# Optimization experiments

Measured on AMD Instinct MI355X. Metric: run time of the kernel, lower is better.

Reference implementation:

```python
import jax, jax.numpy as jnp
import numpy as np

B, S, D, E = 4, 1024, 1024, 4
HID = 2816  # multiple_of * ceil(int(2*4*D/3) / multiple_of), multiple_of=256
COND = 1024  # min(D, 1024)
NORM_EPS = 1e-5  # block norms
LN_EPS = 1e-5    # q_norm/k_norm default eps


def setup_inputs() -> dict:
    key = jax.random.key(0)
    ks = jax.random.split(key, 16)
    w = lambda i, shape: jax.random.normal(ks[i], shape, jnp.float32) * 0.02
    return {
        'x': jax.random.normal(ks[0], (B, S, D), jnp.float32),
        'freqs_cis': jax.random.normal(ks[1], (S, 32), jnp.float32),  # unused by the block
        'adaln_input': jax.random.normal(ks[2], (B, COND), jnp.float32),
        'wq': w(3, (D, D)), 'wk': w(4, (D, D)), 'wv': w(5, (D, D)), 'wo': w(6, (D, D)),
        'q_norm_w': jnp.ones((D,), jnp.float32), 'q_norm_b': jnp.zeros((D,), jnp.float32),
        'k_norm_w': jnp.ones((D,), jnp.float32), 'k_norm_b': jnp.zeros((D,), jnp.float32),
        'attn_norm_w': jnp.ones((D,), jnp.float32), 'attn_norm_b': jnp.zeros((D,), jnp.float32),
        'ffn_norm_w': jnp.ones((D,), jnp.float32), 'ffn_norm_b': jnp.zeros((D,), jnp.float32),
        'w1': w(7, (E, D, HID)), 'w2': w(8, (E, HID, D)), 'w3': w(9, (E, D, HID)),
        'router_w': w(10, (D, E)), 'router_b': jnp.zeros((E,), jnp.float32),
        'ada_w': w(11, (COND, 6 * D)), 'ada_b': jnp.zeros((6 * D,), jnp.float32),
    }


def _ln(x, w, b, eps):
    mu = jnp.mean(x, -1, keepdims=True)
    var = jnp.mean((x - mu) ** 2, -1, keepdims=True)
    return (x - mu) * jax.lax.rsqrt(var + eps) * w + b


def _attention(x, wq, wk, wv, wo, qn_w, qn_b, kn_w, kn_b):
    # NOTE: this module attends over the FEATURE dim (no head split, no 1/sqrt(d) scale):
    # xq,xk,xv are permuted to [B, D, S]; scores are [B, D, D].
    q = _ln(x @ wq, qn_w, qn_b, LN_EPS)
    k = _ln(x @ wk, kn_w, kn_b, LN_EPS)
    v = x @ wv
    scores = jnp.einsum('bsd,bse->bde', q, k)          # [B, D, D]
    attn = jax.nn.softmax(scores, axis=-1)
    out = jnp.einsum('bde,bse->bsd', attn, v)          # [B, S, D]
    return out @ wo


def _moe(x, w1, w2, w3, router_w, router_b):
    logits = x @ router_w + router_b                   # [B, S, E]
    # F.normalize default dim=1 -> L2-normalize along the SEQUENCE dim (faithful quirk)
    nrm = jnp.sqrt(jnp.sum(logits * logits, axis=1, keepdims=True))
    logits = logits / jnp.maximum(nrm, 1e-12)
    probs = jax.nn.softmax(logits, axis=-1)
    topw, topi = jax.lax.top_k(probs, 2)
    # dense combine weights [B,S,E]: identical math to the masked gather/scatter dispatch
    combine = jnp.sum(jax.nn.one_hot(topi, E, dtype=x.dtype) * topw[..., None], axis=-2)
    h1 = jnp.einsum('bsd,edh->ebsh', x, w1)
    h3 = jnp.einsum('bsd,edh->ebsh', x, w3)
    out_e = jnp.einsum('ebsh,ehd->ebsd', jnp.sin(h1) * h3, w2)
    moe = jnp.einsum('bse,ebsd->bsd', combine, out_e)
    avg = jnp.mean(probs, axis=0)                      # [S, E] (mean over batch dim only)
    aux = jnp.sum((1.0 / E - avg) ** 2)
    return moe, aux


def reference(x, freqs_cis, adaln_input, wq, wk, wv, wo, q_norm_w, q_norm_b, k_norm_w,
              k_norm_b, attn_norm_w, attn_norm_b, ffn_norm_w, ffn_norm_b, w1, w2, w3,
              router_w, router_b, ada_w, ada_b):
    ada = jax.nn.silu(adaln_input) @ ada_w + ada_b     # [B, 6D]
    shift_msa, scale_msa, gate_msa, shift_mlp, scale_mlp, gate_mlp = jnp.split(ada, 6, axis=1)
    h = _ln(x, attn_norm_w, attn_norm_b, NORM_EPS)
    h = h * (1.0 + scale_msa[:, None, :]) + shift_msa[:, None, :]
    x = x + gate_msa[:, None, :] * _attention(h, wq, wk, wv, wo, q_norm_w, q_norm_b, k_norm_w, k_norm_b)
    h = _ln(x, ffn_norm_w, ffn_norm_b, NORM_EPS)
    h = h * (1.0 + scale_mlp[:, None, :]) + shift_mlp[:, None, :]
    # MoE path REPLACES x (no residual, gate_mlp unused) — faithful to the source
    x, aux = _moe(h, w1, w2, w3, router_w, router_b)
    return x, aux
```

## Files before the change

kernel.cpp:

```cpp
#include <hip/hip_runtime.h>
#include <hip/hip_bf16.h>
#include <math.h>

#define BB 4
#define SS 1024
#define DD 1024
#define EE 4
#define HID 2816
#define HC 1408
#define SIXD 6144
#define NSLOT 8704
#define NMB 68

typedef __bf16 v8bf __attribute__((ext_vector_type(8)));
typedef float  v4f  __attribute__((ext_vector_type(4)));

__device__ __forceinline__ ushort f2bf(float f) {
    union { float f; unsigned u; } v; v.f = f;
    unsigned r = v.u + 0x7fff + ((v.u >> 16) & 1);
    return (ushort)(r >> 16);
}
__device__ __forceinline__ float bf2f(ushort u) {
    union { unsigned u; float f; } v; v.u = ((unsigned)u) << 16;
    return v.f;
}
__device__ __forceinline__ void split_bf(float x, ushort& h, ushort& l) {
    h = f2bf(x);
    l = f2bf(x - bf2f(h));
}
__device__ __forceinline__ void gload16(const void* g, void* l) {
    __builtin_amdgcn_global_load_lds((const __attribute__((address_space(1))) void*)g,
                                     (__attribute__((address_space(3))) void*)l, 16, 0, 0);
}
template<int N> __device__ __forceinline__ void wait_vm() {
    __builtin_amdgcn_s_waitcnt((N & 15) | (0x7 << 4) | (0xF << 8) | ((N >> 4) << 14));
}

__device__ __forceinline__ void xcd_remap(int& bx, int& by) {
    const int gx = gridDim.x, gy = gridDim.y;
    const int nwg = gx * gy;
    const int wid = bx + gx * by;
    const int q = nwg >> 3, r = nwg & 7;
    const int xcd = wid & 7, loc = wid >> 3;
    const int pos = (xcd < r) ? (xcd * (q + 1) + loc)
                              : (r * (q + 1) + (xcd - r) * q + loc);
    bx = pos % gx; by = pos / gx;
}

__device__ __forceinline__ void xcd_remap_cm(int& bx, int& by) {
    const int gx = gridDim.x, gy = gridDim.y;
    const int nwg = gx * gy;
    const int wid = bx + gx * by;
    const int q = nwg >> 3, r = nwg & 7;
    const int xcd = wid & 7, loc = wid >> 3;
    const int pos = (xcd < r) ? (xcd * (q + 1) + loc)
                              : (r * (q + 1) + (xcd - r) * q + loc);
    bx = pos / gy; by = pos % gy;
}

__device__ __forceinline__ void moe_remap(int& bx, int& by) {
    const int gx = gridDim.x, gy = gridDim.y;
    const int total = gx * gy;
    const int wid = bx + gx * by;
    if ((total & 7) || (gx & 1)) { xcd_remap(bx, by); return; }
    const int q = total >> 3;
    const int pos = (wid & 7) * q + (wid >> 3);
    const int NG = gx >> 1;
    const int gh = NG * gy;
    const int nh = pos / gh, r = pos % gh;
    by = r / NG;
    bx = nh * NG + (r % NG);
}

template<int EPI, bool SPLIT, bool MOE>
__global__ __launch_bounds__(256, 2) void mgemm(
    const ushort* __restrict__ Ah, const ushort* __restrict__ Al,
    const ushort* __restrict__ Bh, const ushort* __restrict__ Bl,
    void* __restrict__ Cv, ushort* __restrict__ C2,
    const float* __restrict__ f1, const float* __restrict__ f2,
    const int* __restrict__ tokidx, const int* __restrict__ mbe,
    const int* __restrict__ mbm,
    int K, int lda, int ldb, int ldc,
    long sA, long sB, long sC)
{
    constexpr int STG = SPLIT ? 12288 : 6144;
    constexpr int BH  = SPLIT ? 8192 : 4096;
    constexpr int L   = SPLIT ? 6 : 3;
    __shared__ __align__(16) ushort smem[3 * STG];

    const int tid  = threadIdx.x;
    const int wv   = tid >> 6, lane = tid & 63;

    int bx = blockIdx.x, by = blockIdx.y;
    if (MOE) moe_remap(bx, by); else xcd_remap(bx, by);
    const int n0 = bx * 64;

    int eexp = 0, m0;
    if (MOE) {
        eexp = mbe[by];
        if (eexp < 0) return;
        m0 = mbm[by];
    } else {
        m0 = by * 128;
    }
    const long zA = MOE ? 0 : (long)blockIdx.z * sA;
    const long zB = MOE ? (long)eexp * sB : (long)blockIdx.z * sB;
    const long zC = MOE ? 0 : (long)blockIdx.z * sC;

    const int lrow = tid >> 2;
    const int skq  = ((tid & 3) ^ ((tid >> 3) & 3)) * 8;
    const int lm   = lane & 15;
    const int qs   = (((lane >> 4) ^ ((lm >> 1) & 3)) * 8);

    v4f acc[2][4];
    const v4f vzero = {0.f, 0.f, 0.f, 0.f};
    #pragma unroll
    for (int i = 0; i < 2; ++i)
        #pragma unroll
        for (int j = 0; j < 4; ++j) acc[i][j] = vzero;

    auto issue = [&](int kt, int st) {
        const long kk = (long)kt * 32 + skq;
        ushort* base = smem + st * STG;
        #pragma unroll
        for (int c = 0; c < 2; ++c) {
            const int row  = c * 64 + lrow;
            const int loff = (c * 64 + wv * 16) * 32;
            gload16(Ah + zA + (long)(m0 + row) * lda + kk, base + loff);
            if (SPLIT)
                gload16(Al + zA + (long)(m0 + row) * lda + kk, base + 4096 + loff);
        }
        {
            const int loff = wv * 16 * 32;
            gload16(Bh + zB + (long)(n0 + lrow) * ldb + kk, base + BH + loff);
            if (SPLIT)
                gload16(Bl + zB + (long)(n0 + lrow) * ldb + kk, base + BH + 2048 + loff);
        }
    };

    const int nk = K / 32;
    issue(0, 0);
    if (nk > 1) issue(1, 1);
    for (int kt = 0; kt < nk; ++kt) {
        if (kt + 1 < nk) wait_vm<L>(); else wait_vm<0>();
        __builtin_amdgcn_s_barrier();
        if (kt + 2 < nk) issue(kt + 2, (kt + 2) % 3);
        const ushort* As = smem + (kt % 3) * STG;
        v8bf a[2], b[4];
        #pragma unroll
        for (int i = 0; i < 2; ++i) a[i] = *(const v8bf*)(As + (wv*32 + 16*i + lm) * 32 + qs);
        #pragma unroll
        for (int j = 0; j < 4; ++j) b[j] = *(const v8bf*)(As + BH + (16*j + lm) * 32 + qs);
        #pragma unroll
        for (int i = 0; i < 2; ++i)
            #pragma unroll
            for (int j = 0; j < 4; ++j)
                acc[i][j] = __builtin_amdgcn_mfma_f32_16x16x32_bf16(a[i], b[j], acc[i][j], 0, 0, 0);
        if (SPLIT) {
            v8bf al[2], bl[4];
            #pragma unroll
            for (int i = 0; i < 2; ++i) al[i] = *(const v8bf*)(As + 4096 + (wv*32 + 16*i + lm) * 32 + qs);
            #pragma unroll
            for (int j = 0; j < 4; ++j) bl[j] = *(const v8bf*)(As + BH + 2048 + (16*j + lm) * 32 + qs);
            #pragma unroll
            for (int i = 0; i < 2; ++i)
                #pragma unroll
                for (int j = 0; j < 4; ++j) {
                    acc[i][j] = __builtin_amdgcn_mfma_f32_16x16x32_bf16(a[i],  bl[j], acc[i][j], 0, 0, 0);
                    acc[i][j] = __builtin_amdgcn_mfma_f32_16x16x32_bf16(al[i], b[j],  acc[i][j], 0, 0, 0);
                }
        }
    }

    const int r0 = (lane >> 4) * 4;
    if (EPI == 7) {
        #pragma unroll
        for (int i = 0; i < 2; ++i)
            #pragma unroll
            for (int r = 0; r < 4; ++r) {
                const int rowg = m0 + wv*32 + 16*i + r0 + r;
                const int t = tokidx[rowg];
                if (t >= 0) {
                    const float cw = f1[t * 4 + eexp];
                    #pragma unroll
                    for (int j = 0; j < 4; ++j)
                        atomicAdd((float*)Cv + (long)t * 1024 + n0 + 16*j + lm, cw * acc[i][j][r]);
                }
            }
    } else {
        #pragma unroll
        for (int i = 0; i < 2; ++i) {
            #pragma unroll
            for (int j = 0; j < 4; ++j) {
                const int colg = n0 + 16*j + lm;
                #pragma unroll
                for (int r = 0; r < 4; ++r) {
                    const long rowg = (long)(m0 + wv*32 + 16*i + r0 + r);
                    const long idx  = zC + rowg * ldc + colg;
                    const float val = acc[i][j][r];
                    if (EPI == 0) {
                        ((float*)Cv)[idx] = val;
                    } else if (EPI == 2) {
                        ((float*)Cv)[idx] = f1[idx] + f2[(rowg >> 10) * SIXD + 2048 + colg] * val;
                    } else if (EPI == 5) {
                        ushort h, l; split_bf(val, h, l);
                        ((ushort*)Cv)[idx] = h;
                        C2[idx] = l;
                    }
                }
            }
        }
    }
}

__global__ __launch_bounds__(256, 2) void mgemm_qkv(
    const ushort* __restrict__ Ah, const ushort* __restrict__ Al,
    const ushort* __restrict__ Bqh, const ushort* __restrict__ Bql,
    const ushort* __restrict__ Bkh, const ushort* __restrict__ Bkl,
    const ushort* __restrict__ Bvh, const ushort* __restrict__ Bvl,
    float* __restrict__ Cq, float* __restrict__ Ck,
    ushort* __restrict__ Cvh, ushort* __restrict__ Cvl)
{
    constexpr int STG = 20480;
    __shared__ __align__(16) ushort smem[2 * STG];

    const int tid  = threadIdx.x;
    const int wv   = tid >> 6, lane = tid & 63;

    int bx = blockIdx.x, by = blockIdx.y;
    xcd_remap(bx, by);
    const int n0 = bx * 64, m0 = by * 128;

    const int lrow = tid >> 2;
    const int skq  = ((tid & 3) ^ ((tid >> 3) & 3)) * 8;
    const int lm   = lane & 15;
    const int qs   = (((lane >> 4) ^ ((lm >> 1) & 3)) * 8);

    const ushort* Bh_[3] = {Bqh, Bkh, Bvh};
    const ushort* Bl_[3] = {Bql, Bkl, Bvl};

    v4f aq[2][4], ak[2][4], av[2][4];
    const v4f vzero = {0.f, 0.f, 0.f, 0.f};
    #pragma unroll
    for (int i = 0; i < 2; ++i)
        #pragma unroll
        for (int j = 0; j < 4; ++j) { aq[i][j] = vzero; ak[i][j] = vzero; av[i][j] = vzero; }

    auto issue = [&](int kt, int st) {
        const long kk = (long)kt * 32 + skq;
        ushort* base = smem + st * STG;
        #pragma unroll
        for (int c = 0; c < 2; ++c) {
            const int row  = c * 64 + lrow;
            const int loff = (c * 64 + wv * 16) * 32;
            gload16(Ah + (long)(m0 + row) * 1024 + kk, base + loff);
            gload16(Al + (long)(m0 + row) * 1024 + kk, base + 4096 + loff);
        }
        const int loff = wv * 16 * 32;
        #pragma unroll
        for (int m = 0; m < 3; ++m) {
            gload16(Bh_[m] + (long)(n0 + lrow) * 1024 + kk, base + 8192 + m * 4096 + loff);
            gload16(Bl_[m] + (long)(n0 + lrow) * 1024 + kk, base + 8192 + m * 4096 + 2048 + loff);
        }
    };

    issue(0, 0);
    #pragma unroll 1
    for (int kt = 0; kt < 32; ++kt) {
        const int stg = kt & 1;
        if (kt) __builtin_amdgcn_s_barrier();
        const bool hasNext = (kt + 1 < 32);
        if (hasNext) issue(kt + 1, stg ^ 1);
        if (hasNext) wait_vm<10>(); else wait_vm<0>();
        __builtin_amdgcn_s_barrier();
        const ushort* As = smem + stg * STG;
        v8bf a[2], alo[2];
        #pragma unroll
        for (int i = 0; i < 2; ++i) {
            a[i]   = *(const v8bf*)(As + (wv*32 + 16*i + lm) * 32 + qs);
            alo[i] = *(const v8bf*)(As + 4096 + (wv*32 + 16*i + lm) * 32 + qs);
        }
        auto mat = [&](const ushort* Bs, v4f (&acc)[2][4]) {
            v8bf b[4], bl[4];
            #pragma unroll
            for (int j = 0; j < 4; ++j) {
                b[j]  = *(const v8bf*)(Bs + (16*j + lm) * 32 + qs);
                bl[j] = *(const v8bf*)(Bs + 2048 + (16*j + lm) * 32 + qs);
            }
            #pragma unroll
            for (int i = 0; i < 2; ++i)
                #pragma unroll
                for (int j = 0; j < 4; ++j) {
                    acc[i][j] = __builtin_amdgcn_mfma_f32_16x16x32_bf16(a[i],   b[j],  acc[i][j], 0, 0, 0);
                    acc[i][j] = __builtin_amdgcn_mfma_f32_16x16x32_bf16(a[i],   bl[j], acc[i][j], 0, 0, 0);
                    acc[i][j] = __builtin_amdgcn_mfma_f32_16x16x32_bf16(alo[i], b[j],  acc[i][j], 0, 0, 0);
                }
        };
        mat(As + 8192,        aq);
        mat(As + 8192 + 4096, ak);
        mat(As + 8192 + 8192, av);
    }

    const int r0 = (lane >> 4) * 4;
    #pragma unroll
    for (int i = 0; i < 2; ++i)
        #pragma unroll
        for (int j = 0; j < 4; ++j) {
            const int colg = n0 + 16*j + lm;
            #pragma unroll
            for (int r = 0; r < 4; ++r) {
                const long rowg = (long)(m0 + wv*32 + 16*i + r0 + r);
                const long idx  = rowg * 1024 + colg;
                Cq[idx] = aq[i][j][r];
                Ck[idx] = ak[i][j][r];
                ushort h, l; split_bf(av[i][j][r], h, l);
                Cvh[idx] = h;
                Cvl[idx] = l;
            }
        }
}

__global__ __launch_bounds__(512, 2) void mgemm_h1h3(
    const ushort* __restrict__ Ah, const ushort* __restrict__ B1,
    const ushort* __restrict__ B2, ushort* __restrict__ Cb,
    const int* __restrict__ tokidx, const int* __restrict__ mbe,
    const int* __restrict__ mbm, long sB)
{
    constexpr int STG = 12288;
    __shared__ __align__(16) ushort smem[3 * STG];

    const int tid  = threadIdx.x;
    const int wv   = tid >> 6, lane = tid & 63;
    const int wr   = wv >> 2, wc = wv & 3;

    int bx = blockIdx.x, by = blockIdx.y;
    xcd_remap_cm(bx, by);
    const int n0 = bx * 128;
    const int eexp = mbe[by];
    if (eexp < 0) return;
    const int m0 = mbm[by];
    const long zB = (long)eexp * sB;

    const int lrow = tid >> 2;
    const int skq  = ((tid & 3) ^ ((tid >> 3) & 3)) * 8;
    const int lm   = lane & 15;
    const int qs   = (((lane >> 4) ^ ((lm >> 1) & 3)) * 8);

    const int t = tokidx[m0 + lrow];
    const long arow = (t < 0) ? 0 : (long)t;

    v4f acc[4][2], acc2[4][2];
    const v4f vzero = {0.f, 0.f, 0.f, 0.f};
    #pragma unroll
    for (int i = 0; i < 4; ++i)
        #pragma unroll
        for (int j = 0; j < 2; ++j) { acc[i][j] = vzero; acc2[i][j] = vzero; }

    auto issue = [&](int kt, int st) {
        const long kk = (long)kt * 32 + skq;
        ushort* base = smem + st * STG;
        const int loff = wv * 16 * 32;
        gload16(Ah + arow * 1024 + kk, base + loff);
        gload16(B1 + zB + (long)(n0 + lrow) * 1024 + kk, base + 4096 + loff);
        gload16(B2 + zB + (long)(n0 + lrow) * 1024 + kk, base + 8192 + loff);
    };

    issue(0, 0);
    issue(1, 1);
    int s_cur = 0, s_nxt = 2;
    #pragma unroll 1
    for (int kt = 0; kt < 32; ++kt) {
        if (kt + 1 < 32) wait_vm<3>(); else wait_vm<0>();
        __builtin_amdgcn_s_barrier();
        if (kt + 2 < 32) issue(kt + 2, s_nxt);
        const ushort* As = smem + s_cur * STG;
        v8bf a[4], b1[2], b2[2];
        #pragma unroll
        for (int i = 0; i < 4; ++i) a[i] = *(const v8bf*)(As + (wr*64 + 16*i + lm) * 32 + qs);
        #pragma unroll
        for (int j = 0; j < 2; ++j) {
            b1[j] = *(const v8bf*)(As + 4096 + (wc*32 + 16*j + lm) * 32 + qs);
            b2[j] = *(const v8bf*)(As + 8192 + (wc*32 + 16*j + lm) * 32 + qs);
        }
        #pragma unroll
        for (int i = 0; i < 4; ++i)
            #pragma unroll
            for (int j = 0; j < 2; ++j) {
                acc[i][j]  = __builtin_amdgcn_mfma_f32_16x16x32_bf16(a[i], b1[j], acc[i][j],  0, 0, 0);
                acc2[i][j] = __builtin_amdgcn_mfma_f32_16x16x32_bf16(a[i], b2[j], acc2[i][j], 0, 0, 0);
            }
        s_cur = (s_cur == 2) ? 0 : s_cur + 1;
        s_nxt = (s_nxt == 2) ? 0 : s_nxt + 1;
    }

    const int r0 = (lane >> 4) * 4;
    #pragma unroll
    for (int i = 0; i < 4; ++i)
        #pragma unroll
        for (int j = 0; j < 2; ++j) {
            const int colg = n0 + wc*32 + 16*j + lm;
            #pragma unroll
            for (int r = 0; r < 4; ++r) {
                const long rowg = (long)(m0 + wr*64 + 16*i + r0 + r);
                Cb[rowg * HC + colg] = f2bf(sinf(acc[i][j][r]) * acc2[i][j][r]);
            }
        }
}

template<bool SP>
__global__ __launch_bounds__(256) void transp(
    const float* __restrict__ in, ushort* __restrict__ oh, ushort* __restrict__ ol,
    int ldin, int ldout, long sIn, long sOut)
{
    __shared__ float T[64][65];
    const int n0 = blockIdx.x * 64, k0 = blockIdx.y * 64;
    in += (long)blockIdx.z * sIn;
    oh += (long)blockIdx.z * sOut;
    if (SP) ol += (long)blockIdx.z * sOut;
    const int t = threadIdx.x;
    const int rr = t >> 4, c4 = (t & 15) * 4;
    #pragma unroll
    for (int p = 0; p < 4; ++p) {
        const int r = rr + p * 16;
        const float4 v = *(const float4*)(in + (long)(k0 + r) * ldin + n0 + c4);
        T[c4+0][r] = v.x; T[c4+1][r] = v.y; T[c4+2][r] = v.z; T[c4+3][r] = v.w;
    }
    __syncthreads();
    #pragma unroll
    for (int p = 0; p < 4; ++p) {
        const int idx = t + 256 * p;
        const int n = idx >> 4, c = (idx & 15) * 4;
        ushort4 wh, wl;
        float x0 = T[n][c], x1 = T[n][c+1], x2 = T[n][c+2], x3 = T[n][c+3];
        if (SP) {
            split_bf(x0, wh.x, wl.x); split_bf(x1, wh.y, wl.y);
            split_bf(x2, wh.z, wl.z); split_bf(x3, wh.w, wl.w);
        } else {
            wh.x = f2bf(x0); wh.y = f2bf(x1); wh.z = f2bf(x2); wh.w = f2bf(x3);
        }
        *(ushort4*)(oh + (long)(n0 + n) * ldout + k0 + c) = wh;
        if (SP) *(ushort4*)(ol + (long)(n0 + n) * ldout + k0 + c) = wl;
    }
}

__global__ __launch_bounds__(256) void ada_kernel(
    const float* __restrict__ adaln, const float* __restrict__ aw,
    const float* __restrict__ ab, float* __restrict__ ada)
{
    __shared__ float s[DD];
    const int b = blockIdx.y;
    const int tid = threadIdx.x;
    for (int i = tid; i < DD; i += 256) {
        const float v = adaln[(long)b * DD + i];
        s[i] = v / (1.f + expf(-v));
    }
    __syncthreads();
    const int n = blockIdx.x * 256 + tid;
    float acc = 0.f;
    for (int k = 0; k < DD; ++k) acc += s[k] * aw[(long)k * SIXD + n];
    ada[(long)b * SIXD + n] = acc + ab[n];
}

template<int OUT, bool MOD>
__global__ __launch_bounds__(256) void ln_kernel(
    const float* __restrict__ x, const float* __restrict__ w, const float* __restrict__ bias,
    const float* __restrict__ ada, int scale_off, int shift_off,
    float* __restrict__ o32, ushort* __restrict__ oh, ushort* __restrict__ ol, float eps)
{
    const int row = blockIdx.x;
    const int b = row >> 10;
    const int tid = threadIdx.x;
    const float* xr = x + (long)row * DD;
    float v[4]; float s = 0.f, q = 0.f;
    #pragma unroll
    for (int i = 0; i < 4; ++i) { v[i] = xr[tid + 256*i]; s += v[i]; q += v[i]*v[i]; }
    __shared__ float rs_[256], rq_[256];
    rs_[tid] = s; rq_[tid] = q; __syncthreads();
    for (int off = 128; off > 0; off >>= 1) {
        if (tid < off) { rs_[tid] += rs_[tid+off]; rq_[tid] += rq_[tid+off]; }
        __syncthreads();
    }
    const float mu  = rs_[0] * (1.f/DD);
    const float var = rq_[0] * (1.f/DD) - mu*mu;
    const float rstd = rsqrtf(var + eps);
    const float* ar = ada + (long)b * SIXD;
    #pragma unroll
    for (int i = 0; i < 4; ++i) {
        const int d = tid + 256*i;
        float y = (v[i] - mu) * rstd * w[d] + bias[d];
        if (MOD) y = y * (1.f + ar[scale_off + d]) + ar[shift_off + d];
        const long idx = (long)row * DD + d;
        if (OUT == 0) o32[idx] = y;
        else if (OUT == 1) { ushort h, l; split_bf(y, h, l); oh[idx] = h; ol[idx] = l; }
        else oh[idx] = f2bf(y);
    }
}

__global__ __launch_bounds__(256) void softmax_split(
    const float* __restrict__ in, ushort* __restrict__ oh, ushort* __restrict__ ol)
{
    const long row = blockIdx.x;
    const float* p = in + row * 1024;
    const int tid = threadIdx.x;
    float v[4]; float mx = -INFINITY;
    #pragma unroll
    for (int i = 0; i < 4; ++i) { v[i] = p[tid + 256*i]; mx = fmaxf(mx, v[i]); }
    __shared__ float red[256];
    red[tid] = mx; __syncthreads();
    for (int off = 128; off > 0; off >>= 1) {
        if (tid < off) red[tid] = fmaxf(red[tid], red[tid+off]);
        __syncthreads();
    }
    const float rowmax = red[0];
    __syncthreads();
    float s = 0.f;
    #pragma unroll
    for (int i = 0; i < 4; ++i) { v[i] = expf(v[i] - rowmax); s += v[i]; }
    red[tid] = s; __syncthreads();
    for (int off = 128; off > 0; off >>= 1) {
        if (tid < off) red[tid] += red[tid+off];
        __syncthreads();
    }
    const float inv = 1.f / red[0];
    #pragma unroll
    for (int i = 0; i < 4; ++i) {
        ushort h, l; split_bf(v[i] * inv, h, l);
        oh[row*1024 + tid + 256*i] = h;
        ol[row*1024 + tid + 256*i] = l;
    }
}

__global__ __launch_bounds__(256) void ln_router(
    const float* __restrict__ x2, const float* __restrict__ fw, const float* __restrict__ fb,
    const float* __restrict__ ada, const float* __restrict__ rw, const float* __restrict__ rb,
    float* __restrict__ logits, ushort* __restrict__ oh)
{
    const int row = blockIdx.x;
    const int b = row >> 10;
    const int tid = threadIdx.x;
    const float* xr = x2 + (long)row * DD;
    float v[4]; float s = 0.f, q = 0.f;
    #pragma unroll
    for (int i = 0; i < 4; ++i) { v[i] = xr[tid + 256*i]; s += v[i]; q += v[i]*v[i]; }
    __shared__ float rs_[256], rq_[256];
    rs_[tid] = s; rq_[tid] = q; __syncthreads();
    for (int off = 128; off > 0; off >>= 1) {
        if (tid < off) { rs_[tid] += rs_[tid+off]; rq_[tid] += rq_[tid+off]; }
        __syncthreads();
    }
    const float mu  = rs_[0] * (1.f/DD);
    const float var = rq_[0] * (1.f/DD) - mu*mu;
    const float rstd = rsqrtf(var + 1e-5f);
    const float* ar = ada + (long)b * SIXD;
    float acc[4] = {0.f, 0.f, 0.f, 0.f};
    #pragma unroll
    for (int i = 0; i < 4; ++i) {
        const int d = tid + 256*i;
        float h = (v[i] - mu) * rstd * fw[d] + fb[d];
        h = h * (1.f + ar[4096 + d]) + ar[3072 + d];
        oh[(long)row * DD + d] = f2bf(h);
        const float* r4 = rw + (long)d * 4;
        acc[0] += h*r4[0]; acc[1] += h*r4[1]; acc[2] += h*r4[2]; acc[3] += h*r4[3];
    }
    __syncthreads();
    __shared__ float red[256];
    for (int e = 0; e < EE; ++e) {
        red[tid] = acc[e]; __syncthreads();
        for (int off = 128; off > 0; off >>= 1) {
            if (tid < off) red[tid] += red[tid+off];
            __syncthreads();
        }
        if (tid == 0) logits[(long)row * EE + e] = red[0] + rb[e];
        __syncthreads();
    }
}

__global__ __launch_bounds__(1024) void router_all(
    const float* __restrict__ logits, float* __restrict__ comb,
    float* __restrict__ auxout, int* __restrict__ tokidx,
    int* __restrict__ mbe, int* __restrict__ mbm)
{
    __shared__ float pl[16384];
    __shared__ float red[1024];
    __shared__ float nrm_l[16];
    __shared__ int lc[4], loff[4], lpos[4];
    const int tid = threadIdx.x;
    const int wv = tid >> 6, ln = tid & 63;
    {
        const int b = wv >> 2, e = wv & 3;
        float s = 0.f;
        for (int it = 0; it < 16; ++it) {
            const float v = logits[(((long)b << 10) + ln + (it << 6)) * 4 + e];
            s += v * v;
        }
        for (int off = 32; off > 0; off >>= 1) s += __shfl_down(s, off, 64);
        if (ln == 0) nrm_l[wv] = fmaxf(sqrtf(s), 1e-12f);
    }
    if (tid < 4) lc[tid] = 0;
    __syncthreads();
    float cloc[4][4];
    const int rbase = tid * 4;
    for (int rr = 0; rr < 4; ++rr) {
        const int row = rbase + rr;
        const int b = row >> 10;
        float l[4], p[4];
        #pragma unroll
        for (int e = 0; e < 4; ++e) l[e] = logits[(long)row*4 + e] / nrm_l[b*4 + e];
        const float mx = fmaxf(fmaxf(l[0], l[1]), fmaxf(l[2], l[3]));
        float s = 0.f;
        #pragma unroll
        for (int e = 0; e < 4; ++e) { p[e] = expf(l[e] - mx); s += p[e]; }
        const float inv = 1.f / s;
        #pragma unroll
        for (int e = 0; e < 4; ++e) { p[e] *= inv; pl[row*4 + e] = p[e]; }
        int i1 = 0;
        #pragma unroll
        for (int e = 1; e < 4; ++e) if (p[e] > p[i1]) i1 = e;
        int i2 = (i1 == 0) ? 1 : 0;
        #pragma unroll
        for (int e = 0; e < 4; ++e) if (e != i1 && p[e] > p[i2]) i2 = e;
        #pragma unroll
        for (int e = 0; e < 4; ++e) {
            const float c = (e == i1) ? p[i1] : ((e == i2) ? p[i2] : 0.f);
            cloc[rr][e] = c;
            comb[(long)row*4 + e] = c;
            if (c > 0.f) atomicAdd(&lc[e], 1);
        }
    }
    __syncthreads();
    float acc = 0.f;
    for (int i = tid; i < 4096; i += 1024) {
        const int s = i >> 2, e = i & 3;
        const float avg = 0.25f * (pl[s*4+e] + pl[(1024+s)*4+e] +
                                   pl[(2048+s)*4+e] + pl[(3072+s)*4+e]);
        const float d = 0.25f - avg;
        acc += d * d;
    }
    red[tid] = acc; __syncthreads();
    for (int off = 512; off > 0; off >>= 1) {
        if (tid < off) red[tid] += red[tid+off];
        __syncthreads();
    }
    if (tid == 0) auxout[0] = red[0];
    if (tid == 0) {
        int off0 = 0, nb = 0;
        for (int e = 0; e < 4; ++e) {
            loff[e] = off0; lpos[e] = 0;
            const int mb = (lc[e] + 127) >> 7;
            for (int k = 0; k < mb; ++k) { mbe[nb] = e; mbm[nb] = off0 + k*128; ++nb; }
            off0 += mb << 7;
        }
        for (; nb < NMB; ++nb) { mbe[nb] = -1; mbm[nb] = 0; }
    }
    for (int i = tid; i < NSLOT; i += 1024) tokidx[i] = -1;
    __syncthreads();
    for (int rr = 0; rr < 4; ++rr) {
        const int row = rbase + rr;
        #pragma unroll
        for (int e = 0; e < 4; ++e)
            if (cloc[rr][e] > 0.f) {
                const int s = atomicAdd(&lpos[e], 1);
                tokidx[loff[e] + s] = row;
            }
    }
}

__global__ __launch_bounds__(256) void zero_kernel(float4* __restrict__ out)
{
    out[(long)blockIdx.x * 256 + threadIdx.x] = float4{0.f, 0.f, 0.f, 0.f};
}

extern "C" void kernel_launch(void* const* d_in, const int* in_sizes, int n_in,
                              void* d_out, int out_size, void* d_ws, size_t ws_size,
                              hipStream_t stream)
{
    (void)in_sizes; (void)n_in; (void)out_size; (void)ws_size;
    const float* x     = (const float*)d_in[0];
    const float* adaln = (const float*)d_in[2];
    const float* wq    = (const float*)d_in[3];
    const float* wk    = (const float*)d_in[4];
    const float* wv    = (const float*)d_in[5];
    const float* wo    = (const float*)d_in[6];
    const float* qn_w  = (const float*)d_in[7];
    const float* qn_b  = (const float*)d_in[8];
    const float* kn_w  = (const float*)d_in[9];
    const float* kn_b  = (const float*)d_in[10];
    const float* an_w  = (const float*)d_in[11];
    const float* an_b  = (const float*)d_in[12];
    const float* fn_w  = (const float*)d_in[13];
    const float* fn_b  = (const float*)d_in[14];
    const float* w1    = (const float*)d_in[15];
    const float* w2    = (const float*)d_in[16];
    const float* w3    = (const float*)d_in[17];
    const float* rw    = (const float*)d_in[18];
    const float* rb    = (const float*)d_in[19];
    const float* aw    = (const float*)d_in[20];
    const float* ab    = (const float*)d_in[21];
    float* out = (float*)d_out;

    const long NBAT = (long)SS * DD;
    const long NBUF = (long)BB * SS * DD;
#define MB(x) ((long)(x) * 1048576L)

    char* P = (char*)d_ws;
    float* ada    = (float*)P;
    float* logits = (float*)(P + 98304);
    float* comb   = logits + 16384;
    int*   tokidx = (int*)(comb + 16384);
    int*   mbe    = tokidx + NSLOT;
    int*   mbm    = mbe + NMB;

    char* A0 = P + MB(1);
    ushort* wqT_h = (ushort*)(A0 + MB(0));  ushort* wqT_l = (ushort*)(A0 + MB(2));
    ushort* wkT_h = (ushort*)(A0 + MB(4));  ushort* wkT_l = (ushort*)(A0 + MB(6));
    ushort* wvT_h = (ushort*)(A0 + MB(8));  ushort* wvT_l = (ushort*)(A0 + MB(10));
    ushort* woT_h = (ushort*)(A0 + MB(0));  ushort* woT_l = (ushort*)(A0 + MB(2));
    ushort* w1Tc  = (ushort*)(A0 + MB(0));
    ushort* h_h   = (ushort*)(A0 + MB(12)); ushort* h_l  = (ushort*)(A0 + MB(20));
    ushort* qT_h  = (ushort*)(A0 + MB(12)); ushort* qT_l = (ushort*)(A0 + MB(20));
    ushort* ao_h  = (ushort*)(A0 + MB(12)); ushort* ao_l = (ushort*)(A0 + MB(20));
    ushort* actb  = (ushort*)(A0 + MB(12));
    float*  q32   = (float*) (A0 + MB(28));
    float*  sc    = (float*) (A0 + MB(28));
    float*  x2    = (float*) (A0 + MB(28));
    ushort* v_h   = (ushort*)(A0 + MB(44)); ushort* v_l  = (ushort*)(A0 + MB(52));
    float*  k32   = (float*) (A0 + MB(60));
    ushort* at_h  = (ushort*)(A0 + MB(60)); ushort* at_l = (ushort*)(A0 + MB(68));
    ushort* w3Tc  = (ushort*)(A0 + MB(60));
    ushort* kT_h  = (ushort*)(A0 + MB(76)); ushort* kT_l = (ushort*)(A0 + MB(84));
    ushort* h2bf  = (ushort*)(A0 + MB(76));
    ushort* w2Tc  = (ushort*)(A0 + MB(84));

    const dim3 blk(256);

    ada_kernel<<<dim3(SIXD/256, BB), blk, 0, stream>>>(adaln, aw, ab, ada);

    transp<true><<<dim3(16,16,1), blk, 0, stream>>>(wq, wqT_h, wqT_l, 1024, 1024, 0, 0);
    transp<true><<<dim3(16,16,1), blk, 0, stream>>>(wk, wkT_h, wkT_l, 1024, 1024, 0, 0);
    transp<true><<<dim3(16,16,1), blk, 0, stream>>>(wv, wvT_h, wvT_l, 1024, 1024, 0, 0);

    ln_kernel<1,true><<<4096, blk, 0, stream>>>(x, an_w, an_b, ada, 1024, 0,
                                                nullptr, h_h, h_l, 1e-5f);

    mgemm_qkv<<<dim3(16,32), blk, 0, stream>>>(
        h_h, h_l, wqT_h, wqT_l, wkT_h, wkT_l, wvT_h, wvT_l,
        q32, k32, v_h, v_l);

    ln_kernel<0,false><<<4096, blk, 0, stream>>>(q32, qn_w, qn_b, ada, 0, 0, q32, nullptr, nullptr, 1e-5f);
    transp<true><<<dim3(16,16,BB), blk, 0, stream>>>(q32, qT_h, qT_l, 1024, 1024, NBAT, NBAT);

    ln_kernel<0,false><<<4096, blk, 0, stream>>>(k32, kn_w, kn_b, ada, 0, 0, k32, nullptr, nullptr, 1e-5f);
    transp<true><<<dim3(16,16,BB), blk, 0, stream>>>(k32, kT_h, kT_l, 1024, 1024, NBAT, NBAT);

    transp<true><<<dim3(16,16,1), blk, 0, stream>>>(wo, woT_h, woT_l, 1024, 1024, 0, 0);

    mgemm<0,true,false><<<dim3(16,8,BB), blk, 0, stream>>>(
        qT_h, qT_l, kT_h, kT_l, sc, nullptr, nullptr, nullptr, nullptr, nullptr, nullptr,
        1024, 1024, 1024, 1024, NBAT, NBAT, NBAT);

    softmax_split<<<4096, blk, 0, stream>>>(sc, at_h, at_l);

    mgemm<5,true,false><<<dim3(16,8,BB), blk, 0, stream>>>(
        v_h, v_l, at_h, at_l, ao_h, ao_l, nullptr, nullptr, nullptr, nullptr, nullptr,
        1024, 1024, 1024, 1024, NBAT, NBAT, NBAT);

    mgemm<2,true,false><<<dim3(16,32,1), blk, 0, stream>>>(
        ao_h, ao_l, woT_h, woT_l, x2, nullptr, x, ada, nullptr, nullptr, nullptr,
        1024, 1024, 1024, 1024, 0, 0, 0);

    ln_router<<<4096, blk, 0, stream>>>(x2, fn_w, fn_b, ada, rw, rb, logits, h2bf);

    router_all<<<1, dim3(1024), 0, stream>>>(logits, comb, out + NBUF, tokidx, mbe, mbm);
    zero_kernel<<<dim3(4096), blk, 0, stream>>>((float4*)out);

    for (int c = 0; c < HID/HC; ++c) {
        transp<false><<<dim3(22,16,4), blk, 0, stream>>>(
            w1 + (long)c*HC, w1Tc, nullptr, HID, 1024, (long)DD*HID, (long)HC*1024);
        transp<false><<<dim3(22,16,4), blk, 0, stream>>>(
            w3 + (long)c*HC, w3Tc, nullptr, HID, 1024, (long)DD*HID, (long)HC*1024);
        transp<false><<<dim3(16,22,4), blk, 0, stream>>>(
            w2 + (long)c*HC*DD, w2Tc, nullptr, DD, HC, (long)HID*DD, (long)DD*HC);
        mgemm_h1h3<<<dim3(11, NMB), dim3(512), 0, stream>>>(
            h2bf, w1Tc, w3Tc, actb, tokidx, mbe, mbm, (long)HC*1024);
        mgemm<7,false,true><<<dim3(16, NMB), blk, 0, stream>>>(
            actb, nullptr, w2Tc, nullptr, out, nullptr, comb, nullptr, tokidx, mbe, mbm,
            HC, HC, HC, 1024, 0, (long)DD*HC, 0);
    }
#undef MB
}
```

Baseline: 810.6 us.

## Add dedicated 128x128-tile MoE down-projection GEMM kernel

Moves the MoE w2 down-projection out of the generic templated mgemm (128x64 tiles) into a new mgemm_w2 kernel with 128x128 output tiles, a 2x2 wave layout and 4x4 MFMA accumulators per wave. The larger tile raises arithmetic intensity and halves the number of column blocks, so A-tile reloads of the activation rows drop. The generic mgemm loses its MOE path and the atomic-add epilogue. Costs are more accumulator registers per thread and fewer blocks in the grid, which may lower occupancy.

```diff
diff --git a/kernel.cpp b/kernel.cpp
--- a/kernel.cpp
+++ b/kernel.cpp
@@ -72,14 +72,12 @@
     bx = nh * NG + (r % NG);
 }
 
-template<int EPI, bool SPLIT, bool MOE>
+template<int EPI, bool SPLIT>
 __global__ __launch_bounds__(256, 2) void mgemm(
     const ushort* __restrict__ Ah, const ushort* __restrict__ Al,
     const ushort* __restrict__ Bh, const ushort* __restrict__ Bl,
     void* __restrict__ Cv, ushort* __restrict__ C2,
     const float* __restrict__ f1, const float* __restrict__ f2,
-    const int* __restrict__ tokidx, const int* __restrict__ mbe,
-    const int* __restrict__ mbm,
     int K, int lda, int ldb, int ldc,
     long sA, long sB, long sC)
 {
@@ -92,20 +90,12 @@
     const int wv   = tid >> 6, lane = tid & 63;
 
     int bx = blockIdx.x, by = blockIdx.y;
-    if (MOE) moe_remap(bx, by); else xcd_remap(bx, by);
+    xcd_remap(bx, by);
     const int n0 = bx * 64;
-
-    int eexp = 0, m0;
-    if (MOE) {
-        eexp = mbe[by];
-        if (eexp < 0) return;
-        m0 = mbm[by];
-    } else {
-        m0 = by * 128;
-    }
-    const long zA = MOE ? 0 : (long)blockIdx.z * sA;
-    const long zB = MOE ? (long)eexp * sB : (long)blockIdx.z * sB;
-    const long zC = MOE ? 0 : (long)blockIdx.z * sC;
+    const int m0 = by * 128;
+    const long zA = (long)blockIdx.z * sA;
+    const long zB = (long)blockIdx.z * sB;
+    const long zC = (long)blockIdx.z * sC;
 
     const int lrow = tid >> 2;
     const int skq  = ((tid & 3) ^ ((tid >> 3) & 3)) * 8;
@@ -173,40 +163,24 @@
     }
 
     const int r0 = (lane >> 4) * 4;
-    if (EPI == 7) {
-        #pragma unroll
-        for (int i = 0; i < 2; ++i)
+    #pragma unroll
+    for (int i = 0; i < 2; ++i) {
+        #pragma unroll
+        for (int j = 0; j < 4; ++j) {
+            const int colg = n0 + 16*j + lm;
             #pragma unroll
             for (int r = 0; r < 4; ++r) {
-                const int rowg = m0 + wv*32 + 16*i + r0 + r;
-                const int t = tokidx[rowg];
-                if (t >= 0) {
-                    const float cw = f1[t * 4 + eexp];
-                    #pragma unroll
-                    for (int j = 0; j < 4; ++j)
-                        atomicAdd((float*)Cv + (long)t * 1024 + n0 + 16*j + lm, cw * acc[i][j][r]);
-                }
-            }
-    } else {
-        #pragma unroll
-        for (int i = 0; i < 2; ++i) {
-            #pragma unroll
-            for (int j = 0; j < 4; ++j) {
-                const int colg = n0 + 16*j + lm;
-                #pragma unroll
-                for (int r = 0; r < 4; ++r) {
-                    const long rowg = (long)(m0 + wv*32 + 16*i + r0 + r);
-                    const long idx  = zC + rowg * ldc + colg;
-                    const float val = acc[i][j][r];
-                    if (EPI == 0) {
-                        ((float*)Cv)[idx] = val;
-                    } else if (EPI == 2) {
-                        ((float*)Cv)[idx] = f1[idx] + f2[(rowg >> 10) * SIXD + 2048 + colg] * val;
-                    } else if (EPI == 5) {
-                        ushort h, l; split_bf(val, h, l);
-                        ((ushort*)Cv)[idx] = h;
-                        C2[idx] = l;
-                    }
+                const long rowg = (long)(m0 + wv*32 + 16*i + r0 + r);
+                const long idx  = zC + rowg * ldc + colg;
+                const float val = acc[i][j][r];
+                if (EPI == 0) {
+                    ((float*)Cv)[idx] = val;
+                } else if (EPI == 2) {
+                    ((float*)Cv)[idx] = f1[idx] + f2[(rowg >> 10) * SIXD + 2048 + colg] * val;
+                } else if (EPI == 5) {
+                    ushort h, l; split_bf(val, h, l);
+                    ((ushort*)Cv)[idx] = h;
+                    C2[idx] = l;
                 }
             }
         }
@@ -403,6 +377,90 @@
             for (int r = 0; r < 4; ++r) {
                 const long rowg = (long)(m0 + wr*64 + 16*i + r0 + r);
                 Cb[rowg * HC + colg] = f2bf(sinf(acc[i][j][r]) * acc2[i][j][r]);
+            }
+        }
+}
+
+__global__ __launch_bounds__(256, 2) void mgemm_w2(
+    const ushort* __restrict__ Ah, const ushort* __restrict__ Bh,
+    float* __restrict__ Cv, const float* __restrict__ comb,
+    const int* __restrict__ tokidx, const int* __restrict__ mbe,
+    const int* __restrict__ mbm, long sB)
+{
+    constexpr int STG = 8192;
+    __shared__ __align__(16) ushort smem[3 * STG];
+
+    const int tid  = threadIdx.x;
+    const int wv   = tid >> 6, lane = tid & 63;
+    const int wr   = wv >> 1, wc = wv & 1;
+
+    int bx = blockIdx.x, by = blockIdx.y;
+    moe_remap(bx, by);
+    const int n0 = bx * 128;
+    const int eexp = mbe[by];
+    if (eexp < 0) return;
+    const int m0 = mbm[by];
+    const long zB = (long)eexp * sB;
+
+    const int lrow = tid >> 2;
+    const int skq  = ((tid & 3) ^ ((tid >> 3) & 3)) * 8;
+    const int lm   = lane & 15;
+    const int qs   = (((lane >> 4) ^ ((lm >> 1) & 3)) * 8);
+
+    v4f acc[4][4];
+    const v4f vzero = {0.f, 0.f, 0.f, 0.f};
+    #pragma unroll
+    for (int i = 0; i < 4; ++i)
+        #pragma unroll
+        for (int j = 0; j < 4; ++j) acc[i][j] = vzero;
+
+    auto issue = [&](int kt, int st) {
+        const long kk = (long)kt * 32 + skq;
+        ushort* base = smem + st * STG;
+        #pragma unroll
+        for (int c = 0; c < 2; ++c) {
+            const int loff = (c * 64 + wv * 16) * 32;
+            gload16(Ah + (long)(m0 + c * 64 + lrow) * HC + kk, base + loff);
+            gload16(Bh + zB + (long)(n0 + c * 64 + lrow) * HC + kk, base + 4096 + loff);
+        }
+    };
+
+    const int nk = HC / 32;
+    issue(0, 0);
+    issue(1, 1);
+    int s_cur = 0, s_nxt = 2;
+    #pragma unroll 1
+    for (int kt = 0; kt < nk; ++kt) {
+        if (kt + 1 < nk) wait_vm<4>(); else wait_vm<0>();
+        __builtin_amdgcn_s_barrier();
+        if (kt + 2 < nk) issue(kt + 2, s_nxt);
+        const ushort* As = smem + s_cur * STG;
+        v8bf a[4], b[4];
+        #pragma unroll
+        for (int i = 0; i < 4; ++i) a[i] = *(const v8bf*)(As + (wr*64 + 16*i + lm) * 32 + qs);
+        #pragma unroll
+        for (int j = 0; j < 4; ++j) b[j] = *(const v8bf*)(As + 4096 + (wc*64 + 16*j + lm) * 32 + qs);
+        #pragma unroll
+        for (int i = 0; i < 4; ++i)
+            #pragma unroll
+            for (int j = 0; j < 4; ++j)
+                acc[i][j] = __builtin_amdgcn_mfma_f32_16x16x32_bf16(a[i], b[j], acc[i][j], 0, 0, 0);
+        s_cur = (s_cur == 2) ? 0 : s_cur + 1;
+        s_nxt = (s_nxt == 2) ? 0 : s_nxt + 1;
+    }
+
+    const int r0 = (lane >> 4) * 4;
+    #pragma unroll
+    for (int i = 0; i < 4; ++i)
+        #pragma unroll
+        for (int r = 0; r < 4; ++r) {
+            const int rowg = m0 + wr*64 + 16*i + r0 + r;
+            const int t = tokidx[rowg];
+            if (t >= 0) {
+                const float cw = comb[t * 4 + eexp];
+                #pragma unroll
+                for (int j = 0; j < 4; ++j)
+                    atomicAdd(Cv + (long)t * 1024 + n0 + wc*64 + 16*j + lm, cw * acc[i][j][r]);
             }
         }
 }
@@ -754,18 +812,18 @@
 
     transp<true><<<dim3(16,16,1), blk, 0, stream>>>(wo, woT_h, woT_l, 1024, 1024, 0, 0);
 
-    mgemm<0,true,false><<<dim3(16,8,BB), blk, 0, stream>>>(
-        qT_h, qT_l, kT_h, kT_l, sc, nullptr, nullptr, nullptr, nullptr, nullptr, nullptr,
+    mgemm<0,true><<<dim3(16,8,BB), blk, 0, stream>>>(
+        qT_h, qT_l, kT_h, kT_l, sc, nullptr, nullptr, nullptr,
         1024, 1024, 1024, 1024, NBAT, NBAT, NBAT);
 
     softmax_split<<<4096, blk, 0, stream>>>(sc, at_h, at_l);
 
-    mgemm<5,true,false><<<dim3(16,8,BB), blk, 0, stream>>>(
-        v_h, v_l, at_h, at_l, ao_h, ao_l, nullptr, nullptr, nullptr, nullptr, nullptr,
+    mgemm<5,true><<<dim3(16,8,BB), blk, 0, stream>>>(
+        v_h, v_l, at_h, at_l, ao_h, ao_l, nullptr, nullptr,
         1024, 1024, 1024, 1024, NBAT, NBAT, NBAT);
 
-    mgemm<2,true,false><<<dim3(16,32,1), blk, 0, stream>>>(
-        ao_h, ao_l, woT_h, woT_l, x2, nullptr, x, ada, nullptr, nullptr, nullptr,
+    mgemm<2,true><<<dim3(16,32,1), blk, 0, stream>>>(
+        ao_h, ao_l, woT_h, woT_l, x2, nullptr, x, ada,
         1024, 1024, 1024, 1024, 0, 0, 0);
 
     ln_router<<<4096, blk, 0, stream>>>(x2, fn_w, fn_b, ada, rw, rb, logits, h2bf);
@@ -782,9 +840,8 @@
             w2 + (long)c*HC*DD, w2Tc, nullptr, DD, HC, (long)HID*DD, (long)DD*HC);
         mgemm_h1h3<<<dim3(11, NMB), dim3(512), 0, stream>>>(
             h2bf, w1Tc, w3Tc, actb, tokidx, mbe, mbm, (long)HC*1024);
-        mgemm<7,false,true><<<dim3(16, NMB), blk, 0, stream>>>(
-            actb, nullptr, w2Tc, nullptr, out, nullptr, comb, nullptr, tokidx, mbe, mbm,
-            HC, HC, HC, 1024, 0, (long)DD*HC, 0);
+        mgemm_w2<<<dim3(8, NMB), blk, 0, stream>>>(
+            actb, w2Tc, out, comb, tokidx, mbe, mbm, (long)DD*HC);
     }
 #undef MB
 }
```

Measured after the change: 814.7 us. Within noise of the previous version (+0.5%).
